# Performance work log

Hardware: AMD Instinct MI355X
Metric: run time of the kernel (lower is better)

## Reference

```python
import jax, jax.numpy as jnp
import numpy as np
import math

NUM_HEADS = 4
PH, PW = 8, 8

def setup_inputs() -> dict:
    key = jax.random.key(0)
    ks = jax.random.split(key, 12)
    B, C, H, W = 2, 128, 256, 256
    x = jax.random.normal(ks[0], (B, C, H, W), dtype=jnp.float32)
    mask = jax.random.uniform(ks[1], (B, 1, H, W), dtype=jnp.float32)
    s1 = 1.0 / math.sqrt(C)          # kaiming-ish scale for 1x1 convs
    s3 = 1.0 / math.sqrt(C * 9)      # 3x3 conv
    wq = jax.random.normal(ks[2], (C, C), dtype=jnp.float32) * s1
    bq = jax.random.normal(ks[3], (C,), dtype=jnp.float32) * 0.01
    wk = jax.random.normal(ks[4], (C, C), dtype=jnp.float32) * s1
    bk = jax.random.normal(ks[5], (C,), dtype=jnp.float32) * 0.01
    wv = jax.random.normal(ks[6], (C, C), dtype=jnp.float32) * s1
    bv = jax.random.normal(ks[7], (C,), dtype=jnp.float32) * 0.01
    wo = jax.random.normal(ks[8], (C, C, 3, 3), dtype=jnp.float32) * s3
    bo = jax.random.normal(ks[9], (C,), dtype=jnp.float32) * 0.01
    return {"x": x, "mask": mask, "wq": wq, "bq": bq, "wk": wk, "bk": bk,
            "wv": wv, "bv": bv, "wo": wo, "bo": bo}

def _conv1x1(x, w, b):
    # w: [O, I]; x: [B, C, H, W]
    return jnp.einsum('oc,bchw->bohw', w, x) + b[None, :, None, None]

def _window(t, b, heads, dph, out_h, out_w):
    # [B, C, H, W] -> [B, heads, out_h*out_w, dph*PH*PW]
    t = t.reshape(b, heads, dph, out_h, PH, out_w, PW)
    t = t.transpose(0, 1, 3, 5, 2, 4, 6)
    return t.reshape(b, heads, out_h * out_w, dph * PH * PW)

def reference(x, mask, wq, bq, wk, bk, wv, bv, wo, bo):
    b, c, h, w = x.shape
    heads = NUM_HEADS
    dph = c // heads
    out_h, out_w = h // PH, w // PW
    d = dph * PH * PW

    q = _window(_conv1x1(x, wq, bq), b, heads, dph, out_h, out_w)
    k = _window(_conv1x1(x, wk, bk), b, heads, dph, out_h, out_w)
    v = _window(_conv1x1(x, wv, bv), b, heads, dph, out_h, out_w)

    # NOTE: original torch code calls att.masked_fill(mask, -1e9) without
    # assignment (not in-place), so the mask has no effect on the output.
    att = jnp.einsum('bhqd,bhkd->bhqk', q, k) * (1.0 / math.sqrt(d))
    p = jax.nn.softmax(att, axis=-1)
    y = jnp.einsum('bhqk,bhkd->bhqd', p, v)

    # un-window: [B, heads, S, d] -> [B, C, H, W]
    y = y.reshape(b, heads, out_h, out_w, dph, PH, PW)
    y = y.transpose(0, 1, 4, 2, 5, 3, 6).reshape(b, c, h, w)

    # output: reflect-padded 3x3 conv + LeakyReLU(0.2)
    yp = jnp.pad(y, ((0, 0), (0, 0), (1, 1), (1, 1)), mode='reflect')
    out = jax.lax.conv_general_dilated(
        yp, wo, window_strides=(1, 1), padding='VALID',
        dimension_numbers=('NCHW', 'OIHW', 'NCHW')) + bo[None, :, None, None]
    return jnp.where(out > 0, out, 0.2 * out)
```

## Files before the change

### kernel.cpp

```cpp
#include <hip/hip_runtime.h>
#include <hip/hip_bf16.h>
#include <stdint.h>

typedef unsigned short u16;
typedef __attribute__((ext_vector_type(8))) short bf16x8;
typedef __attribute__((ext_vector_type(4))) short bf16x4;
typedef __attribute__((ext_vector_type(4))) float f32x4;
typedef __attribute__((ext_vector_type(4))) unsigned short u16x4;

__device__ __forceinline__ float bf2f(u16 u) {
  union { unsigned i; float f; } c; c.i = ((unsigned)u) << 16; return c.f;
}
__device__ __forceinline__ u16 f2bf(float f) {
  union { float f; unsigned i; } c; c.f = f;
  unsigned r = c.i + 0x7FFFu + ((c.i >> 16) & 1u);
  return (u16)(r >> 16);
}
__device__ __forceinline__ void gl2lds16(const u16* g, u16* l) {
  __builtin_amdgcn_global_load_lds(
      (const __attribute__((address_space(1))) unsigned int*)(uintptr_t)g,
      (__attribute__((address_space(3))) unsigned int*)(uintptr_t)l,
      16, 0, 0);
}

__global__ void k_prep(const float* __restrict__ wo, const float* __restrict__ wq,
                       const float* __restrict__ wk, const float* __restrict__ wv,
                       u16* __restrict__ WT, u16* __restrict__ WQKV) {
  int i = blockIdx.x * 256 + threadIdx.x;
  if (i < 9 * 128 * 128) {
    int c = i & 127;
    int o = (i >> 7) & 127;
    int tap = i >> 14;
    WT[i] = f2bf(wo[((o * 128 + c) * 3 + tap / 3) * 3 + tap % 3]);
  } else {
    int j = i - 9 * 128 * 128;
    if (j < 3 * 16384) {
      int sel = j >> 14, rest = j & 16383;
      const float* w = sel == 0 ? wq : (sel == 1 ? wk : wv);
      WQKV[j] = f2bf(w[rest]);
    }
  }
}

__global__ __launch_bounds__(256) void k_qkv(
    const float* __restrict__ x, const u16* __restrict__ WQKV,
    const float* __restrict__ bq, const float* __restrict__ bk,
    const float* __restrict__ bv,
    u16* __restrict__ Q, u16* __restrict__ K, u16* __restrict__ V) {
  const int blk = blockIdx.x;
  const int b = blk >> 9;
  const int t = blk & 511;
  const int th = t & 31, tw = t >> 5;
  const int h0 = th * 8, w0 = tw * 16;
  const int s0 = th * 32 + tw * 2;
  const int tid = threadIdx.x, lane = tid & 63, wid = tid >> 6;
  const int wr = wid >> 1, wc = wid & 1;
  const int g = lane >> 4, l15 = lane & 15;

  __shared__ u16 Xt[128 * 136];
  __shared__ u16 Ot[64 * 136];

  #pragma unroll
  for (int j = 0; j < 8; ++j) {
    int lin = j * 256 + tid;
    int c = lin >> 4;
    int ci = lin & 15;
    int lh = ci >> 1, lw8 = (ci & 1) * 8;
    const float* src = x + (size_t)b * 8388608 + (size_t)c * 65536 + (h0 + lh) * 256 + w0 + lw8;
    float4 v0 = *(const float4*)src;
    float4 v1 = *(const float4*)(src + 4);
    int px = lh * 16 + lw8;
    int ch = c >> 3;
    int chp = (ch & 8) | ((ch & 7) ^ ((px >> 3) & 7));
    u16* dst = &Xt[px * 136 + chp * 8 + (c & 7)];
    dst[0 * 136] = f2bf(v0.x); dst[1 * 136] = f2bf(v0.y);
    dst[2 * 136] = f2bf(v0.z); dst[3 * 136] = f2bf(v0.w);
    dst[4 * 136] = f2bf(v1.x); dst[5 * 136] = f2bf(v1.y);
    dst[6 * 136] = f2bf(v1.z); dst[7 * 136] = f2bf(v1.w);
  }
  __syncthreads();

  for (int sel = 0; sel < 3; ++sel) {
    const u16* w = WQKV + sel * 16384;
    const float* bias = sel == 0 ? bq : (sel == 1 ? bk : bv);
    u16* qkv = sel == 0 ? Q : (sel == 1 ? K : V);

    f32x4 acc[4][4] = {};
    #pragma unroll
    for (int k0 = 0; k0 < 128; k0 += 32) {
      bf16x8 a[4], bb[4];
      #pragma unroll
      for (int m = 0; m < 4; ++m) {
        int o = wr * 64 + m * 16 + l15;
        a[m] = *(const bf16x8*)(w + o * 128 + k0 + g * 8);
      }
      #pragma unroll
      for (int n = 0; n < 4; ++n) {
        int p = wc * 64 + n * 16 + l15;
        int ch = (k0 >> 3) + g;
        int chp = (ch & 8) | ((ch & 7) ^ ((p >> 3) & 7));
        bb[n] = *(const bf16x8*)&Xt[p * 136 + chp * 8];
      }
      #pragma unroll
      for (int m = 0; m < 4; ++m)
        #pragma unroll
        for (int n = 0; n < 4; ++n)
          acc[m][n] = __builtin_amdgcn_mfma_f32_16x16x32_bf16(a[m], bb[n], acc[m][n], 0, 0, 0);
    }

    float4 bias4[4];
    #pragma unroll
    for (int m = 0; m < 4; ++m)
      bias4[m] = *(const float4*)&bias[wr * 64 + m * 16 + g * 4];

    #pragma unroll
    for (int h2 = 0; h2 < 2; ++h2) {
      __syncthreads();
      if (wc == h2) {
        #pragma unroll
        for (int m = 0; m < 4; ++m) {
          int o0 = wr * 64 + m * 16 + g * 4;
          #pragma unroll
          for (int n = 0; n < 4; ++n) {
            int p = n * 16 + l15;
            u16x4 pk = { f2bf(acc[m][n][0] + bias4[m].x),
                         f2bf(acc[m][n][1] + bias4[m].y),
                         f2bf(acc[m][n][2] + bias4[m].z),
                         f2bf(acc[m][n][3] + bias4[m].w) };
            *(u16x4*)&Ot[p * 136 + o0] = pk;
          }
        }
      }
      __syncthreads();
      #pragma unroll
      for (int it = 0; it < 4; ++it) {
        int ci = it * 256 + tid;
        int hs = ci >> 7;
        int rem = ci & 127;
        int head = hs >> 1, s2 = hs & 1;
        int pixw = h2 * 32 + (rem >> 2);
        int dphc = rem & 3;
        int pl = (pixw >> 3) * 16 + s2 * 8 + (pixw & 7) - h2 * 64;
        bf16x8 vv = *(const bf16x8*)&Ot[pl * 136 + head * 32 + dphc * 8];
        size_t gaddr = ((size_t)((b * 4 + head) * 1024 + s0 + s2)) * 2048 + pixw * 32 + dphc * 8;
        *(bf16x8*)(qkv + gaddr) = vv;
      }
    }
  }
}

__global__ __launch_bounds__(256) void k_qk(const u16* __restrict__ Q,
                                            const u16* __restrict__ K,
                                            float* __restrict__ ATT) {
  const int bh = blockIdx.x & 7;
  const int tile = blockIdx.x >> 3;
  const int tm = tile & 7, tn = tile >> 3;
  const int row0 = tm * 128, col0 = tn * 128;
  const int tid = threadIdx.x, lane = tid & 63, wid = tid >> 6;
  const int wr = wid >> 1, wc = wid & 1;
  __shared__ u16 As[128 * 32];
  __shared__ u16 Bs[128 * 32];
  const u16* Ab = Q + (size_t)bh * 1024 * 2048 + (size_t)row0 * 2048;
  const u16* Bb = K + (size_t)bh * 1024 * 2048 + (size_t)col0 * 2048;
  f32x4 acc[4][4] = {};
  const int lr = lane >> 2, lc = lane & 3;
  const int scs = lc ^ ((lr >> 1) & 3);
  const int rsw = ((lane & 15) >> 1) & 3;

  for (int k0 = 0; k0 < 2048; k0 += 32) {
    __syncthreads();
    const u16* s0 = Ab + (size_t)(wid * 16 + lr) * 2048 + k0 + scs * 8;
    gl2lds16(s0, &As[wid * 512]);
    gl2lds16(s0 + (size_t)64 * 2048, &As[2048 + wid * 512]);
    const u16* s1 = Bb + (size_t)(wid * 16 + lr) * 2048 + k0 + scs * 8;
    gl2lds16(s1, &Bs[wid * 512]);
    gl2lds16(s1 + (size_t)64 * 2048, &Bs[2048 + wid * 512]);
    asm volatile("s_waitcnt vmcnt(0)" ::: "memory");
    __syncthreads();
    bf16x8 a[4], bb[4];
    const int g = lane >> 4;
    const int chp = (g ^ rsw) * 8;
    #pragma unroll
    for (int m = 0; m < 4; ++m)
      a[m] = *(const bf16x8*)&As[(wr * 64 + m * 16 + (lane & 15)) * 32 + chp];
    #pragma unroll
    for (int n = 0; n < 4; ++n)
      bb[n] = *(const bf16x8*)&Bs[(wc * 64 + n * 16 + (lane & 15)) * 32 + chp];
    #pragma unroll
    for (int m = 0; m < 4; ++m)
      #pragma unroll
      for (int n = 0; n < 4; ++n)
        acc[m][n] = __builtin_amdgcn_mfma_f32_16x16x32_bf16(a[m], bb[n], acc[m][n], 0, 0, 0);
  }
  const float scale = 0.02209708691207961f;
  float* out = ATT + (size_t)bh * 1024 * 1024;
  #pragma unroll
  for (int m = 0; m < 4; ++m) {
    int r = row0 + wr * 64 + m * 16 + ((lane >> 4) << 2);
    #pragma unroll
    for (int n = 0; n < 4; ++n) {
      int cc = col0 + wc * 64 + n * 16 + (lane & 15);
      #pragma unroll
      for (int j = 0; j < 4; ++j)
        out[(size_t)(r + j) * 1024 + cc] = acc[m][n][j] * scale;
    }
  }
}

__global__ __launch_bounds__(256) void k_vt(const u16* __restrict__ V,
                                            u16* __restrict__ VT) {
  const int bh = blockIdx.y;
  const int ts = blockIdx.x & 7, td = blockIdx.x >> 3;
  const int s0 = ts * 128, d0 = td * 128;
  const int tid = threadIdx.x;
  __shared__ u16 T[128 * 128];
  const u16* Vb = V + (size_t)bh * 1024 * 2048 + (size_t)s0 * 2048 + d0;

  #pragma unroll
  for (int pass = 0; pass < 8; ++pass) {
    int r = pass * 16 + (tid >> 4);
    int c8 = (tid & 15) * 8;
    union { uint4 u; u16 e[8]; } d;
    d.u = *(const uint4*)(Vb + (size_t)r * 2048 + c8);
    int chunk = (r >> 3) ^ ((c8 >> 3) & 15);
    u16* dst = &T[0];
    #pragma unroll
    for (int e = 0; e < 8; ++e)
      dst[(c8 + e) * 128 + chunk * 8 + (r & 7)] = d.e[e];
  }
  __syncthreads();
  u16* VTb = VT + (size_t)bh * 2048 * 1024 + (size_t)d0 * 1024 + s0;
  #pragma unroll
  for (int pass = 0; pass < 8; ++pass) {
    int rd = pass * 16 + (tid >> 4);
    int c8 = (tid & 15) * 8;
    int chunk = (c8 >> 3) ^ ((rd >> 3) & 15);
    bf16x8 v = *(const bf16x8*)&T[rd * 128 + chunk * 8];
    *(bf16x8*)(VTb + (size_t)rd * 1024 + c8) = v;
  }
}

__global__ __launch_bounds__(256) void k_softmax(const float* __restrict__ ATT,
                                                 u16* __restrict__ P) {
  const int row = blockIdx.x;
  const float* a = ATT + (size_t)row * 1024;
  const int tid = threadIdx.x;
  float4 v = *(const float4*)(a + tid * 4);
  float mx = fmaxf(fmaxf(v.x, v.y), fmaxf(v.z, v.w));
  #pragma unroll
  for (int off = 32; off; off >>= 1) mx = fmaxf(mx, __shfl_xor(mx, off, 64));
  __shared__ float red[8];
  if ((tid & 63) == 0) red[tid >> 6] = mx;
  __syncthreads();
  mx = fmaxf(fmaxf(red[0], red[1]), fmaxf(red[2], red[3]));
  float e0 = __expf(v.x - mx), e1 = __expf(v.y - mx);
  float e2 = __expf(v.z - mx), e3 = __expf(v.w - mx);
  float s = e0 + e1 + e2 + e3;
  #pragma unroll
  for (int off = 32; off; off >>= 1) s += __shfl_xor(s, off, 64);
  if ((tid & 63) == 0) red[4 + (tid >> 6)] = s;
  __syncthreads();
  s = red[4] + red[5] + red[6] + red[7];
  float inv = 1.0f / s;
  u16x4 o = { f2bf(e0 * inv), f2bf(e1 * inv), f2bf(e2 * inv), f2bf(e3 * inv) };
  *(u16x4*)(P + (size_t)row * 1024 + tid * 4) = o;
}

__global__ __launch_bounds__(256) void k_pv(const u16* __restrict__ P,
                                            const u16* __restrict__ VT,
                                            u16* __restrict__ Yn) {
  const int bh = blockIdx.x & 7;
  const int tile = blockIdx.x >> 3;
  const int tm = tile & 7, tn = tile >> 3;
  const int row0 = tm * 128, col0 = tn * 128;
  const int tid = threadIdx.x, lane = tid & 63, wid = tid >> 6;
  const int wr = wid >> 1, wc = wid & 1;
  __shared__ __align__(16) u16 smem[17408];
  u16* As = smem;
  u16* Bs = smem + 4096;
  u16* Ot = smem;
  const u16* Pb = P + (size_t)bh * 1024 * 1024 + (size_t)row0 * 1024;
  const u16* VTb = VT + (size_t)bh * 2048 * 1024 + (size_t)col0 * 1024;
  f32x4 acc[4][4] = {};
  const int lr = lane >> 2, lc = lane & 3;
  const int scs = lc ^ ((lr >> 1) & 3);
  const int rsw = ((lane & 15) >> 1) & 3;

  for (int k0 = 0; k0 < 1024; k0 += 32) {
    __syncthreads();
    const u16* s0 = Pb + (size_t)(wid * 16 + lr) * 1024 + k0 + scs * 8;
    gl2lds16(s0, &As[wid * 512]);
    gl2lds16(s0 + (size_t)64 * 1024, &As[2048 + wid * 512]);
    const u16* s1 = VTb + (size_t)(wid * 16 + lr) * 1024 + k0 + scs * 8;
    gl2lds16(s1, &Bs[wid * 512]);
    gl2lds16(s1 + (size_t)64 * 1024, &Bs[2048 + wid * 512]);
    asm volatile("s_waitcnt vmcnt(0)" ::: "memory");
    __syncthreads();
    bf16x8 a[4], bb[4];
    const int g = lane >> 4;
    const int chp = (g ^ rsw) * 8;
    #pragma unroll
    for (int m = 0; m < 4; ++m)
      a[m] = *(const bf16x8*)&As[(wr * 64 + m * 16 + (lane & 15)) * 32 + chp];
    #pragma unroll
    for (int n = 0; n < 4; ++n)
      bb[n] = *(const bf16x8*)&Bs[(wc * 64 + n * 16 + (lane & 15)) * 32 + chp];
    #pragma unroll
    for (int m = 0; m < 4; ++m)
      #pragma unroll
      for (int n = 0; n < 4; ++n)
        acc[m][n] = __builtin_amdgcn_mfma_f32_16x16x32_bf16(a[m], bb[n], acc[m][n], 0, 0, 0);
  }

  __syncthreads();
  #pragma unroll
  for (int m = 0; m < 4; ++m) {
    int r0 = wr * 64 + m * 16 + ((lane >> 4) << 2);
    #pragma unroll
    for (int n = 0; n < 4; ++n) {
      int dv = wc * 64 + n * 16 + (lane & 15);
      #pragma unroll
      for (int j = 0; j < 4; ++j)
        Ot[(r0 + j) * 136 + dv] = f2bf(acc[m][n][j]);
    }
  }
  __syncthreads();
  const int b = bh >> 2, head = bh & 3;
  const int pixw0 = tn * 4;
  #pragma unroll
  for (int it = 0; it < 8; ++it) {
    int ci = it * 256 + tid;
    int sl = ci >> 4;
    int pxl = (ci >> 2) & 3;
    int dc = ci & 3;
    bf16x8 vv = *(const bf16x8*)&Ot[sl * 136 + pxl * 32 + dc * 8];
    int s = row0 + sl, oh = s >> 5, ow = s & 31;
    int pixw = pixw0 + pxl, ph = pixw >> 3, pw = pixw & 7;
    int h = oh * 8 + ph, w2 = ow * 8 + pw;
    size_t gaddr = (((size_t)(b * 256 + h) * 256) + w2) * 128 + head * 32 + dc * 8;
    *(bf16x8*)(Yn + gaddr) = vv;
  }
}

__global__ __launch_bounds__(512, 2) void k_conv(const u16* __restrict__ Yn,
                                                 const u16* __restrict__ WT,
                                                 const float* __restrict__ bo,
                                                 float* __restrict__ out) {
  const int wgid = blockIdx.x;
  const int r7 = wgid & 7;
  const int b = (r7 >> 2) & 1;
  const int w0 = ((r7 >> 1) & 1) * 128;
  const int h0 = ((r7 & 1) * 32 + (wgid >> 3)) * 4;
  const int tid = threadIdx.x, lane = tid & 63, wid = tid >> 6;
  const int wo_ = wid & 1;
  const int wh = wid >> 1;
  const int g = lane >> 4, l15 = lane & 15;
  __shared__ u16 S[6][136 * 64];
  f32x4 acc[4][8] = {};

  auto stage = [&](int chalf) {
    for (int g5 = wid; g5 < 102; g5 += 8) {
      int rowi = g5 / 17, grp = g5 % 17;
      int rg = grp * 8 + (lane >> 3);
      int chunk = lane & 7;
      int row = h0 + rowi - 1;
      row = row < 0 ? 1 : (row > 255 ? 254 : row);
      int wsrc = w0 - 1 + rg;
      wsrc = wsrc < 0 ? 1 : (wsrc > 255 ? 254 : wsrc);
      const u16* src = Yn + ((size_t)(b * 256 + row) * 256 + wsrc) * 128 + chalf * 64
                         + ((chunk ^ (rg & 7)) * 8);
      gl2lds16(src, &S[rowi][grp * 512]);
    }
  };

  #pragma unroll
  for (int chalf = 0; chalf < 2; ++chalf) {
    if (chalf) __syncthreads();
    stage(chalf);
    asm volatile("s_waitcnt vmcnt(0)" ::: "memory");
    __syncthreads();
    #pragma unroll
    for (int ky = 0; ky < 3; ++ky) {
      #pragma unroll
      for (int kx = 0; kx < 3; ++kx) {
        const int tap = ky * 3 + kx;
        bf16x8 areg[2][4];
        #pragma unroll
        for (int ckh = 0; ckh < 2; ++ckh)
          #pragma unroll
          for (int m = 0; m < 4; ++m) {
            int o = wo_ * 64 + m * 16 + l15;
            areg[ckh][m] = *(const bf16x8*)(WT + ((size_t)tap * 128 + o) * 128
                                            + chalf * 64 + ckh * 32 + g * 8);
          }
        #pragma unroll
        for (int ckh = 0; ckh < 2; ++ckh) {
          #pragma unroll
          for (int nh = 0; nh < 2; ++nh) {
            bf16x8 bb[4];
            #pragma unroll
            for (int n4 = 0; n4 < 4; ++n4) {
              int p = (nh * 4 + n4) * 16 + l15 + kx;
              int chunk = ((ckh << 2) + g) ^ (p & 7);
              bb[n4] = *(const bf16x8*)&S[wh + ky][p * 64 + chunk * 8];
            }
            #pragma unroll
            for (int m = 0; m < 4; ++m)
              #pragma unroll
              for (int n4 = 0; n4 < 4; ++n4)
                acc[m][nh * 4 + n4] = __builtin_amdgcn_mfma_f32_16x16x32_bf16(
                    areg[ckh][m], bb[n4], acc[m][nh * 4 + n4], 0, 0, 0);
          }
        }
      }
    }
  }
  #pragma unroll
  for (int m = 0; m < 4; ++m) {
    int o0 = wo_ * 64 + m * 16 + (g << 2);
    #pragma unroll
    for (int n = 0; n < 8; ++n) {
      int p = n * 16 + l15;
      #pragma unroll
      for (int j = 0; j < 4; ++j) {
        int o = o0 + j;
        float v = acc[m][n][j] + bo[o];
        v = v > 0.f ? v : 0.2f * v;
        out[(((size_t)b * 128 + o) << 16) + ((h0 + wh) << 8) + w0 + p] = v;
      }
    }
  }
}

extern "C" void kernel_launch(void* const* d_in, const int* in_sizes, int n_in,
                              void* d_out, int out_size, void* d_ws, size_t ws_size,
                              hipStream_t stream) {
  const float* x  = (const float*)d_in[0];
  const float* wq = (const float*)d_in[2];
  const float* bq = (const float*)d_in[3];
  const float* wk = (const float*)d_in[4];
  const float* bk = (const float*)d_in[5];
  const float* wv = (const float*)d_in[6];
  const float* bv = (const float*)d_in[7];
  const float* wo = (const float*)d_in[8];
  const float* bo = (const float*)d_in[9];

  char* ws = (char*)d_ws;
  u16*   WT   = (u16*)(ws);
  u16*   WQKV = (u16*)(ws + (size_t)(512 << 10));
  u16*   Q   = (u16*)(ws + (size_t)(1  << 20));
  u16*   K   = (u16*)(ws + (size_t)(33 << 20));
  u16*   V   = (u16*)(ws + (size_t)(65 << 20));
  float* ATT = (float*)(ws + (size_t)(97 << 20));
  u16*   P   = (u16*)(ws + (size_t)(129 << 20));
  u16*   Yn  = (u16*)(ws + (size_t)(145 << 20));
  u16*   VT  = Q;
  float* outp = (float*)d_out;

  k_prep<<<768, 256, 0, stream>>>(wo, wq, wk, wv, WT, WQKV);
  k_qkv<<<1024, 256, 0, stream>>>(x, WQKV, bq, bk, bv, Q, K, V);
  k_qk<<<512, 256, 0, stream>>>(Q, K, ATT);
  k_vt<<<dim3(128, 8), 256, 0, stream>>>(V, VT);
  k_softmax<<<8192, 256, 0, stream>>>(ATT, P);
  k_pv<<<1024, 256, 0, stream>>>(P, VT, Yn);
  k_conv<<<256, 512, 0, stream>>>(Yn, WT, bo, outp);
}
```

Baseline: 229.2 us.

## Stage conv weights in double-buffered LDS and use packed bf16 conversion

The 3x3 conv kernel now copies each tap's weight slice into a double-buffered LDS array with async global-to-LDS loads. The next tap's slice is prefetched while the current tap's MFMAs run, replacing the per-wave global weight loads. The QKV kernel handles two input channels per thread and converts with the packed v_cvt_pk_bf16_f32 instruction, writing 32-bit LDS words, and its epilogue uses the same packed conversion. The trade-off is a full barrier and vmcnt wait after every tap, plus about 32KB of extra LDS, which may limit occupancy.

Result: faster. 213.5 us (-6.8%).

```diff
diff --git a/kernel.cpp b/kernel.cpp
--- a/kernel.cpp
+++ b/kernel.cpp
@@ -15,6 +15,11 @@
   union { float f; unsigned i; } c; c.f = f;
   unsigned r = c.i + 0x7FFFu + ((c.i >> 16) & 1u);
   return (u16)(r >> 16);
+}
+__device__ __forceinline__ unsigned cvt_pk(float lo, float hi) {
+  unsigned r;
+  asm("v_cvt_pk_bf16_f32 %0, %1, %2" : "=v"(r) : "v"(lo), "v"(hi));
+  return r;
 }
 __device__ __forceinline__ void gl2lds16(const u16* g, u16* l) {
   __builtin_amdgcn_global_load_lds(
@@ -61,22 +66,30 @@
   __shared__ u16 Ot[64 * 136];
 
   #pragma unroll
-  for (int j = 0; j < 8; ++j) {
+  for (int j = 0; j < 4; ++j) {
     int lin = j * 256 + tid;
-    int c = lin >> 4;
+    int c2 = lin >> 4;
     int ci = lin & 15;
+    int c = c2 * 2;
     int lh = ci >> 1, lw8 = (ci & 1) * 8;
-    const float* src = x + (size_t)b * 8388608 + (size_t)c * 65536 + (h0 + lh) * 256 + w0 + lw8;
-    float4 v0 = *(const float4*)src;
-    float4 v1 = *(const float4*)(src + 4);
-    int px = lh * 16 + lw8;
+    const float* s0p = x + (size_t)b * 8388608 + (size_t)c * 65536 + (h0 + lh) * 256 + w0 + lw8;
+    const float* s1p = s0p + 65536;
+    float4 a0 = *(const float4*)s0p;
+    float4 a1 = *(const float4*)(s0p + 4);
+    float4 c0 = *(const float4*)s1p;
+    float4 c1 = *(const float4*)(s1p + 4);
+    int px = ci * 8;
     int ch = c >> 3;
-    int chp = (ch & 8) | ((ch & 7) ^ ((px >> 3) & 7));
-    u16* dst = &Xt[px * 136 + chp * 8 + (c & 7)];
-    dst[0 * 136] = f2bf(v0.x); dst[1 * 136] = f2bf(v0.y);
-    dst[2 * 136] = f2bf(v0.z); dst[3 * 136] = f2bf(v0.w);
-    dst[4 * 136] = f2bf(v1.x); dst[5 * 136] = f2bf(v1.y);
-    dst[6 * 136] = f2bf(v1.z); dst[7 * 136] = f2bf(v1.w);
+    int chp = (ch & 8) | ((ch & 7) ^ (ci & 7));
+    unsigned* dst = (unsigned*)&Xt[px * 136 + chp * 8 + (c & 7)];
+    dst[0 * 68] = cvt_pk(a0.x, c0.x);
+    dst[1 * 68] = cvt_pk(a0.y, c0.y);
+    dst[2 * 68] = cvt_pk(a0.z, c0.z);
+    dst[3 * 68] = cvt_pk(a0.w, c0.w);
+    dst[4 * 68] = cvt_pk(a1.x, c1.x);
+    dst[5 * 68] = cvt_pk(a1.y, c1.y);
+    dst[6 * 68] = cvt_pk(a1.z, c1.z);
+    dst[7 * 68] = cvt_pk(a1.w, c1.w);
   }
   __syncthreads();
 
@@ -123,11 +136,10 @@
           #pragma unroll
           for (int n = 0; n < 4; ++n) {
             int p = n * 16 + l15;
-            u16x4 pk = { f2bf(acc[m][n][0] + bias4[m].x),
-                         f2bf(acc[m][n][1] + bias4[m].y),
-                         f2bf(acc[m][n][2] + bias4[m].z),
-                         f2bf(acc[m][n][3] + bias4[m].w) };
-            *(u16x4*)&Ot[p * 136 + o0] = pk;
+            unsigned r0 = cvt_pk(acc[m][n][0] + bias4[m].x, acc[m][n][1] + bias4[m].y);
+            unsigned r1 = cvt_pk(acc[m][n][2] + bias4[m].z, acc[m][n][3] + bias4[m].w);
+            unsigned* dp = (unsigned*)&Ot[p * 136 + o0];
+            dp[0] = r0; dp[1] = r1;
           }
         }
       }
@@ -356,9 +368,10 @@
   const int wh = wid >> 1;
   const int g = lane >> 4, l15 = lane & 15;
   __shared__ u16 S[6][136 * 64];
+  __shared__ u16 WTl[2][8192];
   f32x4 acc[4][8] = {};
 
-  auto stage = [&](int chalf) {
+  auto stageS = [&](int chalf) {
     for (int g5 = wid; g5 < 102; g5 += 8) {
       int rowi = g5 / 17, grp = g5 % 17;
       int rg = grp * 8 + (lane >> 3);
@@ -372,26 +385,48 @@
       gl2lds16(src, &S[rowi][grp * 512]);
     }
   };
+  auto stageWT = [&](int chalf, int tap, int nb) {
+    #pragma unroll
+    for (int r2 = 0; r2 < 2; ++r2) {
+      int g5 = wid + r2 * 8;
+      int orow = g5 * 8 + (lane >> 3);
+      int csrc = (lane & 7) ^ (lane >> 3);
+      const u16* src = WT + ((size_t)tap * 128 + orow) * 128 + chalf * 64 + csrc * 8;
+      gl2lds16(src, &WTl[nb][g5 * 512]);
+    }
+  };
+
+  int buf = 0;
+  stageS(0);
+  stageWT(0, 0, 0);
+  asm volatile("s_waitcnt vmcnt(0)" ::: "memory");
+  __syncthreads();
 
   #pragma unroll
   for (int chalf = 0; chalf < 2; ++chalf) {
-    if (chalf) __syncthreads();
-    stage(chalf);
-    asm volatile("s_waitcnt vmcnt(0)" ::: "memory");
-    __syncthreads();
+    if (chalf) {
+      __syncthreads();
+      stageS(1);
+      stageWT(1, 0, buf ^ 1);
+      asm volatile("s_waitcnt vmcnt(0)" ::: "memory");
+      __syncthreads();
+      buf ^= 1;
+    }
     #pragma unroll
     for (int ky = 0; ky < 3; ++ky) {
       #pragma unroll
       for (int kx = 0; kx < 3; ++kx) {
         const int tap = ky * 3 + kx;
+        const bool hasNext = (tap < 8);
+        if (hasNext) stageWT(chalf, tap + 1, buf ^ 1);
         bf16x8 areg[2][4];
         #pragma unroll
         for (int ckh = 0; ckh < 2; ++ckh)
           #pragma unroll
           for (int m = 0; m < 4; ++m) {
             int o = wo_ * 64 + m * 16 + l15;
-            areg[ckh][m] = *(const bf16x8*)(WT + ((size_t)tap * 128 + o) * 128
-                                            + chalf * 64 + ckh * 32 + g * 8);
+            int cc2 = ((ckh << 2) + g) ^ (o & 7);
+            areg[ckh][m] = *(const bf16x8*)&WTl[buf][o * 64 + cc2 * 8];
           }
         #pragma unroll
         for (int ckh = 0; ckh < 2; ++ckh) {
@@ -412,6 +447,11 @@
                     areg[ckh][m], bb[n4], acc[m][nh * 4 + n4], 0, 0, 0);
           }
         }
+        if (hasNext) {
+          asm volatile("s_waitcnt vmcnt(0)" ::: "memory");
+          __syncthreads();
+          buf ^= 1;
+        }
       }
     }
   }
```
